# Optimization experiments

Measured on AMD Instinct MI355X. Metric: run time of the kernel, lower is better.

Reference implementation:

```python
import jax, jax.numpy as jnp
import numpy as np

DIM = 1024
NUM_HEADS = 16
HEAD_DIM = DIM // NUM_HEADS


def setup_inputs() -> dict:
    key = jax.random.key(0)
    k1, k2, k3 = jax.random.split(key, 3)
    B, T = 2, 2048
    x = jax.random.normal(k1, (B, T, DIM), dtype=jnp.float32)
    # qkv: Linear(dim, 3*dim, bias=False); torch weight shape [3*dim, dim]
    w_qkv = jax.random.normal(k2, (3 * DIM, DIM), dtype=jnp.float32) * (1.0 / np.sqrt(DIM))
    # out_proj: Linear(dim, dim, bias=False) (zeros in orig init; random for a meaningful baseline)
    w_out = jax.random.normal(k3, (DIM, DIM), dtype=jnp.float32) * (1.0 / np.sqrt(DIM))
    return {"x": x, "w_qkv": w_qkv, "w_out": w_out}


def reference(x, w_qkv, w_out):
    B, T, C = x.shape
    H, D = NUM_HEADS, HEAD_DIM
    qkv = jnp.einsum("btc,fc->btf", x, w_qkv)            # [B,T,3C]
    qkv = qkv.reshape(B, T, 3, H, D).transpose(2, 0, 3, 1, 4)  # [3,B,H,T,D]
    q, k, v = qkv[0], qkv[1], qkv[2]
    scale = 1.0 / np.sqrt(D)
    scores = jnp.einsum("bhtd,bhsd->bhts", q, k) * scale  # [B,H,T,T]
    causal = jnp.tril(jnp.ones((T, T), dtype=bool))
    scores = jnp.where(causal, scores, -jnp.inf)
    attn = jax.nn.softmax(scores, axis=-1)
    out = jnp.einsum("bhts,bhsd->bhtd", attn, v)          # [B,H,T,D]
    out = out.transpose(0, 2, 1, 3).reshape(B, T, C)       # [B,T,C]
    return jnp.einsum("btc,oc->bto", out, w_out)
```

## Files before the change

### kernel.cpp

```cpp
#include <hip/hip_runtime.h>
#include <hip/hip_bf16.h>

typedef __attribute__((ext_vector_type(8))) short vbf8;
typedef __attribute__((ext_vector_type(4))) float vf4;
typedef __attribute__((ext_vector_type(4))) unsigned int vu4;

#define MFMA16(a, b, c) __builtin_amdgcn_mfma_f32_16x16x32_bf16((a), (b), (c), 0, 0, 0)

__device__ __forceinline__ unsigned short f2bf(float f) {
    unsigned int u = __float_as_uint(f);
    u += 0x7fffu + ((u >> 16) & 1u);
    return (unsigned short)(u >> 16);
}

__device__ __forceinline__ unsigned int cvtpk(float a, float b) {
    unsigned int r;
    asm("v_cvt_pk_bf16_f32 %0, %1, %2" : "=v"(r) : "v"(a), "v"(b));
    return r;
}

__device__ __forceinline__ void gload_lds16(const void* g, void* l) {
    __builtin_amdgcn_global_load_lds(
        (const __attribute__((address_space(1))) unsigned int*)(unsigned long long)g,
        (__attribute__((address_space(3))) unsigned int*)(unsigned long long)l,
        16, 0, 0);
}

__global__ __launch_bounds__(256) void cvt_all(
    const float* __restrict__ x, const float* __restrict__ wq, const float* __restrict__ wo,
    unsigned short* __restrict__ xb, unsigned short* __restrict__ wqb, unsigned short* __restrict__ wob)
{
    int i = blockIdx.x * 256 + threadIdx.x;
    const float* src;
    unsigned short* dst;
    int off;
    if (i < 1048576)      { src = x;  dst = xb;  off = i; }
    else if (i < 1835008) { src = wq; dst = wqb; off = i - 1048576; }
    else                  { src = wo; dst = wob; off = i - 1835008; }
    float4 v = ((const float4*)src)[off];
    ushort4 o;
    o.x = f2bf(v.x); o.y = f2bf(v.y); o.z = f2bf(v.z); o.w = f2bf(v.w);
    ((ushort4*)dst)[off] = o;
}

template <int EPI, int NT>
__global__ __launch_bounds__(256) void gemm_bt(
    const unsigned short* __restrict__ A, const unsigned short* __restrict__ Bt,
    int M, int N, int K,
    float* __restrict__ Cf,
    unsigned short* __restrict__ Qo, unsigned short* __restrict__ Ko, unsigned short* __restrict__ Vo)
{
    __shared__ __align__(16) unsigned short sA[128 * 64];
    __shared__ __align__(16) unsigned short sB[NT * 32 * 64];

    const int tid = threadIdx.x;
    const int lane = tid & 63;
    const int w = tid >> 6;
    const int wr = w >> 1, wc = w & 1;
    const int l16 = lane & 15, lhi = lane >> 4;

    const int nbx = gridDim.x;
    const int lin = blockIdx.y * nbx + blockIdx.x;
    const int cpx = (nbx * gridDim.y) >> 3;
    const int swz = (lin & 7) * cpx + (lin >> 3);
    const int bm = swz / nbx, bn = swz % nbx;
    const int row0 = bm * 128, col0 = bn * (NT * 32);

    vf4 acc[4][NT] = {};

    for (int k0 = 0; k0 < K; k0 += 64) {
#pragma unroll
        for (int i = 0; i < 4; ++i) {
            int p = i * 256 + tid;
            int r = p >> 3, cb = p & 7;
            int cs = cb ^ (r & 7);
            gload_lds16(A + (size_t)(row0 + r) * K + k0 + (cs << 3), &sA[p << 3]);
        }
#pragma unroll
        for (int i = 0; i < NT; ++i) {
            int p = i * 256 + tid;
            int r = p >> 3, cb = p & 7;
            int cs = cb ^ (r & 7);
            gload_lds16(Bt + (size_t)(col0 + r) * K + k0 + (cs << 3), &sB[p << 3]);
        }
        __syncthreads();
#pragma unroll
        for (int kk = 0; kk < 2; ++kk) {
            const int cb = kk * 4 + lhi;
            vbf8 af[4], bfr[NT];
#pragma unroll
            for (int mt = 0; mt < 4; ++mt) {
                int r = wr * 64 + mt * 16 + l16;
                af[mt] = *(const vbf8*)&sA[(r << 6) + ((cb ^ (r & 7)) << 3)];
            }
#pragma unroll
            for (int nt = 0; nt < NT; ++nt) {
                int r = wc * (NT * 16) + nt * 16 + l16;
                bfr[nt] = *(const vbf8*)&sB[(r << 6) + ((cb ^ (r & 7)) << 3)];
            }
#pragma unroll
            for (int mt = 0; mt < 4; ++mt)
#pragma unroll
                for (int nt = 0; nt < NT; ++nt)
                    acc[mt][nt] = MFMA16(af[mt], bfr[nt], acc[mt][nt]);
        }
        __syncthreads();
    }

    if (EPI == 0) {
#pragma unroll
        for (int mt = 0; mt < 4; ++mt)
#pragma unroll
            for (int nt = 0; nt < NT; ++nt)
#pragma unroll
                for (int r = 0; r < 4; ++r) {
                    int row = row0 + wr * 64 + mt * 16 + lhi * 4 + r;
                    int col = col0 + wc * (NT * 16) + nt * 16 + l16;
                    Cf[(size_t)row * N + col] = acc[mt][nt][r];
                }
    } else {
        const int which = col0 >> 10;
        const int b = row0 >> 11;
        if (which == 2) {
#pragma unroll
            for (int mt = 0; mt < 4; ++mt)
#pragma unroll
                for (int nt = 0; nt < NT; ++nt) {
                    int row = row0 + wr * 64 + mt * 16 + lhi * 4;
                    int col = col0 + wc * (NT * 16) + nt * 16 + l16;
                    int h = (col >> 6) & 15, d = col & 63;
                    int t = row & 2047;
                    size_t bh = (size_t)(b * 16 + h);
                    ushort4 pv;
                    pv.x = f2bf(acc[mt][nt][0]);
                    pv.y = f2bf(acc[mt][nt][1]);
                    pv.z = f2bf(acc[mt][nt][2]);
                    pv.w = f2bf(acc[mt][nt][3]);
                    *(ushort4*)&Vo[(bh * 64 + d) * 2048 + t] = pv;
                }
        } else {
            unsigned short* dstbuf = (which == 0) ? Qo : Ko;
            const float sc = (which == 0) ? 0.18033688011112042f : 1.0f;
#pragma unroll
            for (int mt = 0; mt < 4; ++mt)
#pragma unroll
                for (int nt = 0; nt < NT; ++nt)
#pragma unroll
                    for (int r = 0; r < 4; ++r) {
                        int row = row0 + wr * 64 + mt * 16 + lhi * 4 + r;
                        int col = col0 + wc * (NT * 16) + nt * 16 + l16;
                        int h = (col >> 6) & 15, d = col & 63;
                        int t = row & 2047;
                        size_t bh = (size_t)(b * 16 + h);
                        dstbuf[(bh * 2048 + t) * 64 + d] = f2bf(acc[mt][nt][r] * sc);
                    }
        }
    }
}

__global__ __launch_bounds__(512, 4) void attn_fwd4(
    const unsigned short* __restrict__ Q, const unsigned short* __restrict__ Kp,
    const unsigned short* __restrict__ Vt, unsigned short* __restrict__ att)
{
    __shared__ __align__(16) unsigned short sK[2][128 * 64];
    __shared__ __align__(16) unsigned short sV[2][64 * 128];

    const int tid = threadIdx.x;
    const int lane = tid & 63;
    const int w = tid >> 6;
    const int l16 = lane & 15, lhi = lane >> 4;
    const int bh = blockIdx.x & 31;
    const int j = blockIdx.x >> 5;
    const int band = (j < 8) ? (15 - j) : (j - 8);
    const size_t hoff = (size_t)bh * 2048 * 64;
    const unsigned short* Qh = Q + hoff;
    const unsigned short* Kh = Kp + hoff;
    const unsigned short* Vh = Vt + hoff;
    const int q0 = band * 128;
    const int qg = q0 + w * 16 + l16;
    const int ktLast = band;

    const int pA = tid, pB = 512 + tid;
    const int rKA = pA >> 3, cKA = pA & 7;
    const int rKB = pB >> 3, cKB = pB & 7;
    const int rVA = pA >> 4, cVA = pA & 15;
    const int rVB = pB >> 4, cVB = pB & 15;
    const unsigned short* pKA = Kh + (size_t)rKA * 64 + ((cKA ^ (rKA & 7)) << 3);
    const unsigned short* pKB = Kh + (size_t)rKB * 64 + ((cKB ^ (rKB & 7)) << 3);
    const unsigned short* pVA = Vh + (size_t)rVA * 2048 + ((cVA ^ (rVA & 7)) << 3);
    const unsigned short* pVB = Vh + (size_t)rVB * 2048 + ((cVB ^ (rVB & 7)) << 3);
    const int dA = pA << 3, dB = pB << 3;

    auto STAGE = [&](int buf, int k0) {
        gload_lds16(pKA + (size_t)k0 * 64, &sK[buf][dA]);
        gload_lds16(pKB + (size_t)k0 * 64, &sK[buf][dB]);
        gload_lds16(pVA + k0, &sV[buf][dA]);
        gload_lds16(pVB + k0, &sV[buf][dB]);
    };

    STAGE(0, 0);

    vbf8 qf[2];
#pragma unroll
    for (int kk = 0; kk < 2; ++kk)
        qf[kk] = *(const vbf8*)&Qh[(size_t)qg * 64 + kk * 32 + lhi * 8];

    vf4 oacc[4] = {};
    float m = -1e30f, lsum = 0.f;

    for (int kt = 0; kt <= ktLast; ++kt) {
        const int cur = kt & 1;
        const int k0 = kt * 128;
        if (kt < ktLast) {
            STAGE(cur ^ 1, k0 + 128);
            asm volatile("s_waitcnt vmcnt(4)" ::: "memory");
        } else {
            asm volatile("s_waitcnt vmcnt(0)" ::: "memory");
        }
        __builtin_amdgcn_s_barrier();
        __builtin_amdgcn_sched_barrier(0);

        const unsigned short* sKc = &sK[cur][0];
        const unsigned short* sVc = &sV[cur][0];

        vf4 sc[8] = {};
#pragma unroll
        for (int kk = 0; kk < 2; ++kk) {
#pragma unroll
            for (int nt = 0; nt < 8; ++nt) {
                int rr = nt * 16 + l16;
                vbf8 kf = *(const vbf8*)&sKc[(rr << 6) + ((((kk << 2) + lhi) ^ (rr & 7)) << 3)];
                sc[nt] = MFMA16(kf, qf[kk], sc[nt]);
            }
        }

        if (kt == ktLast) {
#pragma unroll
            for (int nt = 0; nt < 8; ++nt)
#pragma unroll
                for (int r = 0; r < 4; ++r) {
                    int kg = k0 + nt * 16 + lhi * 4 + r;
                    if (kg > qg) sc[nt][r] = -1e30f;
                }
        }

        float m4[8];
#pragma unroll
        for (int nt = 0; nt < 8; ++nt)
            m4[nt] = fmaxf(fmaxf(sc[nt][0], sc[nt][1]), fmaxf(sc[nt][2], sc[nt][3]));
        float pm = fmaxf(fmaxf(fmaxf(m4[0], m4[1]), fmaxf(m4[2], m4[3])),
                         fmaxf(fmaxf(m4[4], m4[5]), fmaxf(m4[6], m4[7])));
        pm = fmaxf(pm, __shfl_xor(pm, 16, 64));
        pm = fmaxf(pm, __shfl_xor(pm, 32, 64));

        if (!__all(pm - m <= 8.0f)) {
            float mn = fmaxf(m, pm);
            float alpha = exp2f(m - mn);
            lsum *= alpha;
#pragma unroll
            for (int dt = 0; dt < 4; ++dt)
#pragma unroll
                for (int r = 0; r < 4; ++r) oacc[dt][r] *= alpha;
            m = mn;
        }

        float rs4[8];
#pragma unroll
        for (int nt = 0; nt < 8; ++nt) {
#pragma unroll
            for (int r = 0; r < 4; ++r) sc[nt][r] = exp2f(sc[nt][r] - m);
            rs4[nt] = (sc[nt][0] + sc[nt][1]) + (sc[nt][2] + sc[nt][3]);
        }
        float rs = ((rs4[0] + rs4[1]) + (rs4[2] + rs4[3])) +
                   ((rs4[4] + rs4[5]) + (rs4[6] + rs4[7]));
        rs += __shfl_xor(rs, 16, 64);
        rs += __shfl_xor(rs, 32, 64);
        lsum += rs;

        unsigned int pk0[8], pk1[8];
#pragma unroll
        for (int nt = 0; nt < 8; ++nt) {
            pk0[nt] = cvtpk(sc[nt][0], sc[nt][1]);
            pk1[nt] = cvtpk(sc[nt][2], sc[nt][3]);
        }

        const int srcA = l16 + ((lhi & 1) ? 32 : 0);
        const int srcB = srcA + 16;
        const bool hiSel = (lhi >> 1) != 0;
#pragma unroll
        for (int kk = 0; kk < 4; ++kk) {
            unsigned int a0e = __shfl((int)pk0[2 * kk], srcA, 64);
            unsigned int a1e = __shfl((int)pk1[2 * kk], srcA, 64);
            unsigned int b0e = __shfl((int)pk0[2 * kk], srcB, 64);
            unsigned int b1e = __shfl((int)pk1[2 * kk], srcB, 64);
            unsigned int a0o = __shfl((int)pk0[2 * kk + 1], srcA, 64);
            unsigned int a1o = __shfl((int)pk1[2 * kk + 1], srcA, 64);
            unsigned int b0o = __shfl((int)pk0[2 * kk + 1], srcB, 64);
            unsigned int b1o = __shfl((int)pk1[2 * kk + 1], srcB, 64);
            vu4 uw;
            uw.x = hiSel ? a0o : a0e;
            uw.y = hiSel ? a1o : a1e;
            uw.z = hiSel ? b0o : b0e;
            uw.w = hiSel ? b1o : b1e;
            vbf8 pf = __builtin_bit_cast(vbf8, uw);
#pragma unroll
            for (int dt = 0; dt < 4; ++dt) {
                int rr = dt * 16 + l16;
                vbf8 vfr = *(const vbf8*)&sVc[(rr << 7) + ((((kk << 2) + lhi) ^ (rr & 7)) << 3)];
                oacc[dt] = MFMA16(vfr, pf, oacc[dt]);
            }
        }
        __builtin_amdgcn_s_barrier();
        __builtin_amdgcn_sched_barrier(0);
    }

    const float inv = 1.0f / lsum;
    unsigned short* so = &sK[0][0] + w * 1024;
#pragma unroll
    for (int dt = 0; dt < 4; ++dt)
#pragma unroll
        for (int r = 0; r < 4; ++r)
            so[l16 * 64 + (((dt * 2 + (lhi >> 1)) ^ (l16 & 7)) << 3) + (lhi & 1) * 4 + r] =
                f2bf(oacc[dt][r] * inv);
    __syncthreads();

    const int b = bh >> 4, h = bh & 15;
    const int qr = lane >> 2;
    const int cj = lane & 3;
    vbf8 o1 = *(const vbf8*)&so[qr * 64 + (((cj * 2 + 0) ^ (qr & 7)) << 3)];
    vbf8 o2 = *(const vbf8*)&so[qr * 64 + (((cj * 2 + 1) ^ (qr & 7)) << 3)];
    const int qrow = q0 + w * 16 + qr;
    unsigned short* dst = att + ((size_t)(b * 2048 + qrow)) * 1024 + h * 64 + cj * 16;
    *(vbf8*)dst = o1;
    *(vbf8*)(dst + 8) = o2;
}

extern "C" void kernel_launch(void* const* d_in, const int* in_sizes, int n_in,
                              void* d_out, int out_size, void* d_ws, size_t ws_size,
                              hipStream_t stream) {
    const float* x = (const float*)d_in[0];
    const float* w_qkv = (const float*)d_in[1];
    const float* w_out = (const float*)d_in[2];
    float* out = (float*)d_out;

    char* ws = (char*)d_ws;
    unsigned short* xb   = (unsigned short*)(ws);
    unsigned short* wqb  = (unsigned short*)(ws + (8ull << 20));
    unsigned short* wob  = (unsigned short*)(ws + (14ull << 20));
    unsigned short* Qb   = (unsigned short*)(ws + (16ull << 20));
    unsigned short* Kb   = (unsigned short*)(ws + (24ull << 20));
    unsigned short* Vb   = (unsigned short*)(ws + (32ull << 20));
    unsigned short* attb = (unsigned short*)(ws + (40ull << 20));

    cvt_all<<<8192, 256, 0, stream>>>(x, w_qkv, w_out, xb, wqb, wob);

    gemm_bt<1, 4><<<dim3(3072 / 128, 4096 / 128), 256, 0, stream>>>(
        xb, wqb, 4096, 3072, 1024, nullptr, Qb, Kb, Vb);

    attn_fwd4<<<16 * 32, 512, 0, stream>>>(Qb, Kb, Vb, attb);

    gemm_bt<0, 2><<<dim3(1024 / 64, 4096 / 128), 256, 0, stream>>>(
        attb, wob, 4096, 1024, 1024, out, nullptr, nullptr, nullptr);
}
```

Baseline: 105.9 us.

## Replace QKV GEMM with 256x256-tile eight-phase pipelined kernel

Adds a dedicated QKV projection kernel with 256x256 output tiles, 512 threads, and an eight-phase schedule. Each phase computes one 128x128 quadrant while async global-to-LDS loads stage the next K tile into a double buffer, with explicit waitcnt, barriers and setprio around the MFMA blocks. The goal is better data reuse per LDS byte and overlap of global loads with MFMA work. The trade-off is a grid of only 192 blocks and 128 KB of LDS per block, which may underfill the GPU's CUs and adds fragile hand-scheduled synchronisation. The generic GEMM keeps only the fp32 output epilogue for the out-projection.

```diff
diff --git a/kernel.cpp b/kernel.cpp
--- a/kernel.cpp
+++ b/kernel.cpp
@@ -43,12 +43,150 @@
     ((ushort4*)dst)[off] = o;
 }
 
-template <int EPI, int NT>
+__global__ __launch_bounds__(512, 2) void gemm_qkv_8ph(
+    const unsigned short* __restrict__ Ag, const unsigned short* __restrict__ Btg,
+    unsigned short* __restrict__ Qo, unsigned short* __restrict__ Ko, unsigned short* __restrict__ Vo)
+{
+    constexpr int K = 1024;
+    __shared__ __align__(16) unsigned short s[4 * 16384];
+
+    const int tid = threadIdx.x;
+    const int lane = tid & 63;
+    const int w = tid >> 6;
+    const int l16 = lane & 15, lhi = lane >> 4;
+    const int wrow = (w >> 2) * 64;
+    const int wcol = (w & 3) * 32;
+
+    const int nbx = gridDim.x;
+    const int lin = blockIdx.y * nbx + blockIdx.x;
+    const int cpx = (nbx * gridDim.y) >> 3;
+    const int swz = (lin & 7) * cpx + (lin >> 3);
+    const int bm = swz / nbx, bn = swz % nbx;
+    const int row0 = bm * 256, col0 = bn * 256;
+
+    const int rA0 = tid >> 3, cb0 = tid & 7;
+    const unsigned short* srcA = Ag + (size_t)(row0 + rA0) * K + ((cb0 ^ (rA0 & 7)) << 3);
+    const unsigned short* srcB = Btg + (size_t)(col0 + rA0) * K + ((cb0 ^ (rA0 & 7)) << 3);
+    const int dBase = rA0 * 64 + cb0 * 8;
+
+    auto STAGE_A = [&](int b, int h, int kt) {
+        size_t ko = (size_t)((kt & 15) * 64);
+        const unsigned short* g = srcA + (size_t)h * 128 * K + ko;
+        unsigned short* d = s + b * 16384 + h * 8192 + dBase;
+        gload_lds16(g, d);
+        gload_lds16(g + (size_t)64 * K, d + 4096);
+    };
+    auto STAGE_B = [&](int b, int h, int kt) {
+        size_t ko = (size_t)((kt & 15) * 64);
+        const unsigned short* g = srcB + (size_t)h * 128 * K + ko;
+        unsigned short* d = s + 32768 + b * 16384 + h * 8192 + dBase;
+        gload_lds16(g, d);
+        gload_lds16(g + (size_t)64 * K, d + 4096);
+    };
+
+    vf4 acc[2][2][4][2] = {};
+
+    STAGE_A(0, 0, 0); STAGE_B(0, 0, 0); STAGE_A(0, 1, 0); STAGE_B(0, 1, 0);
+    STAGE_A(1, 0, 1); STAGE_B(1, 0, 1);
+    asm volatile("s_waitcnt vmcnt(4)" ::: "memory");
+    __builtin_amdgcn_s_barrier();
+    __builtin_amdgcn_sched_barrier(0);
+
+#define PHASE(RH, CH, BUF, STG, WAIT)                                              \
+    {                                                                              \
+        const unsigned short* sAc = s + (BUF) * 16384;                             \
+        const unsigned short* sBc = s + 32768 + (BUF) * 16384;                     \
+        vbf8 af[4][2], bfv[2][2];                                                  \
+        _Pragma("unroll")                                                          \
+        for (int mt = 0; mt < 4; ++mt)                                             \
+            _Pragma("unroll")                                                      \
+            for (int kk = 0; kk < 2; ++kk) {                                       \
+                int r = (RH) * 128 + wrow + mt * 16 + l16;                         \
+                int cb = kk * 4 + lhi;                                             \
+                af[mt][kk] = *(const vbf8*)&sAc[(r << 6) + ((cb ^ (r & 7)) << 3)]; \
+            }                                                                      \
+        _Pragma("unroll")                                                          \
+        for (int nt = 0; nt < 2; ++nt)                                             \
+            _Pragma("unroll")                                                      \
+            for (int kk = 0; kk < 2; ++kk) {                                       \
+                int r = (CH) * 128 + wcol + nt * 16 + l16;                         \
+                int cb = kk * 4 + lhi;                                             \
+                bfv[nt][kk] = *(const vbf8*)&sBc[(r << 6) + ((cb ^ (r & 7)) << 3)];\
+            }                                                                      \
+        STG;                                                                       \
+        asm volatile("s_waitcnt lgkmcnt(8)" ::: "memory");                         \
+        __builtin_amdgcn_sched_barrier(0);                                         \
+        __builtin_amdgcn_s_barrier();                                              \
+        asm volatile("s_waitcnt lgkmcnt(0)" ::: "memory");                         \
+        __builtin_amdgcn_sched_barrier(0);                                         \
+        __builtin_amdgcn_s_setprio(1);                                             \
+        _Pragma("unroll")                                                          \
+        for (int kk = 0; kk < 2; ++kk)                                             \
+            _Pragma("unroll")                                                      \
+            for (int mt = 0; mt < 4; ++mt)                                         \
+                _Pragma("unroll")                                                  \
+                for (int nt = 0; nt < 2; ++nt)                                     \
+                    acc[RH][CH][mt][nt] =                                          \
+                        MFMA16(af[mt][kk], bfv[nt][kk], acc[RH][CH][mt][nt]);      \
+        __builtin_amdgcn_s_setprio(0);                                             \
+        WAIT;                                                                      \
+        __builtin_amdgcn_s_barrier();                                              \
+        __builtin_amdgcn_sched_barrier(0);                                         \
+    }
+
+#define VMC2 asm volatile("s_waitcnt vmcnt(2)" ::: "memory")
+
+    for (int i = 0; i < 8; ++i) {
+        const int t = 2 * i;
+        PHASE(0, 0, 0, STAGE_A(1, 1, t + 1), )
+        PHASE(0, 1, 0, STAGE_B(1, 1, t + 1), )
+        PHASE(1, 0, 0, STAGE_A(0, 0, t + 2), )
+        PHASE(1, 1, 0, STAGE_B(0, 0, t + 2), VMC2)
+        PHASE(0, 0, 1, STAGE_A(0, 1, t + 2), )
+        PHASE(0, 1, 1, STAGE_B(0, 1, t + 2), )
+        PHASE(1, 0, 1, STAGE_A(1, 0, t + 3), )
+        PHASE(1, 1, 1, STAGE_B(1, 0, t + 3), VMC2)
+    }
+#undef PHASE
+#undef VMC2
+
+    const int which = col0 >> 10;
+    const int b = row0 >> 11;
+#pragma unroll
+    for (int RH = 0; RH < 2; ++RH)
+#pragma unroll
+        for (int CH = 0; CH < 2; ++CH)
+#pragma unroll
+            for (int mt = 0; mt < 4; ++mt)
+#pragma unroll
+                for (int nt = 0; nt < 2; ++nt) {
+                    int rowb = row0 + RH * 128 + wrow + mt * 16 + lhi * 4;
+                    int col = col0 + CH * 128 + wcol + nt * 16 + l16;
+                    int h = (col >> 6) & 15, d = col & 63;
+                    int t = rowb & 2047;
+                    size_t bh = (size_t)(b * 16 + h);
+                    if (which == 2) {
+                        ushort4 pv;
+                        pv.x = f2bf(acc[RH][CH][mt][nt][0]);
+                        pv.y = f2bf(acc[RH][CH][mt][nt][1]);
+                        pv.z = f2bf(acc[RH][CH][mt][nt][2]);
+                        pv.w = f2bf(acc[RH][CH][mt][nt][3]);
+                        *(ushort4*)&Vo[(bh * 64 + d) * 2048 + t] = pv;
+                    } else {
+                        unsigned short* dstbuf = (which == 0) ? Qo : Ko;
+                        const float scq = (which == 0) ? 0.18033688011112042f : 1.0f;
+#pragma unroll
+                        for (int r = 0; r < 4; ++r)
+                            dstbuf[(bh * 2048 + t + r) * 64 + d] =
+                                f2bf(acc[RH][CH][mt][nt][r] * scq);
+                    }
+                }
+}
+
+template <int NT>
 __global__ __launch_bounds__(256) void gemm_bt(
     const unsigned short* __restrict__ A, const unsigned short* __restrict__ Bt,
-    int M, int N, int K,
-    float* __restrict__ Cf,
-    unsigned short* __restrict__ Qo, unsigned short* __restrict__ Ko, unsigned short* __restrict__ Vo)
+    int M, int N, int K, float* __restrict__ Cf)
 {
     __shared__ __align__(16) unsigned short sA[128 * 64];
     __shared__ __align__(16) unsigned short sB[NT * 32 * 64];
@@ -107,55 +245,16 @@
         __syncthreads();
     }
 
-    if (EPI == 0) {
-#pragma unroll
-        for (int mt = 0; mt < 4; ++mt)
-#pragma unroll
-            for (int nt = 0; nt < NT; ++nt)
-#pragma unroll
-                for (int r = 0; r < 4; ++r) {
-                    int row = row0 + wr * 64 + mt * 16 + lhi * 4 + r;
-                    int col = col0 + wc * (NT * 16) + nt * 16 + l16;
-                    Cf[(size_t)row * N + col] = acc[mt][nt][r];
-                }
-    } else {
-        const int which = col0 >> 10;
-        const int b = row0 >> 11;
-        if (which == 2) {
-#pragma unroll
-            for (int mt = 0; mt < 4; ++mt)
-#pragma unroll
-                for (int nt = 0; nt < NT; ++nt) {
-                    int row = row0 + wr * 64 + mt * 16 + lhi * 4;
-                    int col = col0 + wc * (NT * 16) + nt * 16 + l16;
-                    int h = (col >> 6) & 15, d = col & 63;
-                    int t = row & 2047;
-                    size_t bh = (size_t)(b * 16 + h);
-                    ushort4 pv;
-                    pv.x = f2bf(acc[mt][nt][0]);
-                    pv.y = f2bf(acc[mt][nt][1]);
-                    pv.z = f2bf(acc[mt][nt][2]);
-                    pv.w = f2bf(acc[mt][nt][3]);
-                    *(ushort4*)&Vo[(bh * 64 + d) * 2048 + t] = pv;
-                }
-        } else {
-            unsigned short* dstbuf = (which == 0) ? Qo : Ko;
-            const float sc = (which == 0) ? 0.18033688011112042f : 1.0f;
-#pragma unroll
-            for (int mt = 0; mt < 4; ++mt)
-#pragma unroll
-                for (int nt = 0; nt < NT; ++nt)
-#pragma unroll
-                    for (int r = 0; r < 4; ++r) {
-                        int row = row0 + wr * 64 + mt * 16 + lhi * 4 + r;
-                        int col = col0 + wc * (NT * 16) + nt * 16 + l16;
-                        int h = (col >> 6) & 15, d = col & 63;
-                        int t = row & 2047;
-                        size_t bh = (size_t)(b * 16 + h);
-                        dstbuf[(bh * 2048 + t) * 64 + d] = f2bf(acc[mt][nt][r] * sc);
-                    }
-        }
-    }
+#pragma unroll
+    for (int mt = 0; mt < 4; ++mt)
+#pragma unroll
+        for (int nt = 0; nt < NT; ++nt)
+#pragma unroll
+            for (int r = 0; r < 4; ++r) {
+                int row = row0 + wr * 64 + mt * 16 + lhi * 4 + r;
+                int col = col0 + wc * (NT * 16) + nt * 16 + l16;
+                Cf[(size_t)row * N + col] = acc[mt][nt][r];
+            }
 }
 
 __global__ __launch_bounds__(512, 4) void attn_fwd4(
@@ -354,11 +453,11 @@
 
     cvt_all<<<8192, 256, 0, stream>>>(x, w_qkv, w_out, xb, wqb, wob);
 
-    gemm_bt<1, 4><<<dim3(3072 / 128, 4096 / 128), 256, 0, stream>>>(
-        xb, wqb, 4096, 3072, 1024, nullptr, Qb, Kb, Vb);
+    gemm_qkv_8ph<<<dim3(3072 / 256, 4096 / 256), 512, 0, stream>>>(
+        xb, wqb, Qb, Kb, Vb);
 
     attn_fwd4<<<16 * 32, 512, 0, stream>>>(Qb, Kb, Vb, attb);
 
-    gemm_bt<0, 2><<<dim3(1024 / 64, 4096 / 128), 256, 0, stream>>>(
-        attb, wob, 4096, 1024, 1024, out, nullptr, nullptr, nullptr);
-}
+    gemm_bt<2><<<dim3(1024 / 64, 4096 / 128), 256, 0, stream>>>(
+        attb, wob, 4096, 1024, 1024, out);
+}
```

Result: slower. 114.2 us (+7.8%).
